# Optimization experiments

Hardware: AMD Instinct MI355X
Metric: run time of the kernel (lower is better)

Reference implementation:

```python
import jax, jax.numpy as jnp
import numpy as np

B, S, P, E, H = 2, 2048, 2048, 1024, 16
DH = E // H  # 64


def setup_inputs() -> dict:
    key = jax.random.key(0)
    ks = jax.random.split(key, 9)
    query = jax.random.normal(ks[0], (B, S, E), jnp.float32)
    key_in = jax.random.normal(ks[1], (B, S, E), jnp.float32)
    value = jax.random.normal(ks[2], (B, S, E), jnp.float32)
    past_k = jax.random.normal(ks[3], (B, H, P, DH), jnp.float32)
    past_v = jax.random.normal(ks[4], (B, H, P, DH), jnp.float32)
    # additive causal mask over the current block; all past positions visible
    i = jnp.arange(S)[:, None]          # query positions within current block
    j = jnp.arange(P + S)[None, :]      # absolute key positions
    causal = (j <= i + P)
    attn_mask = jnp.where(causal, 0.0, -1e9).astype(jnp.float32)[None, None]  # [1,1,S,P+S]
    sc = 1.0 / np.sqrt(E)
    Wq = jax.random.normal(ks[5], (E, E), jnp.float32) * sc
    Wk = jax.random.normal(ks[6], (E, E), jnp.float32) * sc
    Wv = jax.random.normal(ks[7], (E, E), jnp.float32) * sc
    Wo = jax.random.normal(ks[8], (E, E), jnp.float32) * sc
    return {"query": query, "key": key_in, "value": value,
            "past_k": past_k, "past_v": past_v, "attn_mask": attn_mask,
            "Wq": Wq, "Wk": Wk, "Wv": Wv, "Wo": Wo}


def _split_heads(x):
    # [B, S, E] -> [B, H, S, DH]  (matches view + transpose(1,2))
    b, s, _ = x.shape
    return x.reshape(b, s, H, DH).transpose(0, 2, 1, 3)


def reference(query, key, value, past_k, past_v, attn_mask, Wq, Wk, Wv, Wo):
    q = _split_heads(query @ Wq.T)          # [B,H,S,DH]
    k_new = _split_heads(key @ Wk.T)        # [B,H,S,DH]
    v_new = _split_heads(value @ Wv.T)      # [B,H,S,DH]
    k = jnp.concatenate([past_k, k_new], axis=2)   # [B,H,T,DH], T=P+S
    v = jnp.concatenate([past_v, v_new], axis=2)
    scores = jnp.einsum('bhse,bhte->bhst', q, k) / np.sqrt(DH)
    scores = scores + attn_mask
    attn = jax.nn.softmax(scores, axis=-1)
    out = jnp.einsum('bhst,bhtd->bshd', attn, v)    # [B,S,H,DH]
    out = out.reshape(query.shape[0], -1, E)         # [B,S,E]
    return out @ Wo.T
```

## Files before the change

kernel.cpp:

```cpp
#include <hip/hip_runtime.h>

#define BB 2
#define SS 2048
#define PP 2048
#define TT 4096
#define EE 1024
#define HH 16
#define DH 64

typedef __attribute__((ext_vector_type(8))) __bf16 bf16x8;
typedef __attribute__((ext_vector_type(4))) __bf16 bf16x4;
typedef __attribute__((ext_vector_type(4))) float f32x4;
typedef __attribute__((ext_vector_type(16))) float f32x16;

__device__ __forceinline__ void gload_lds16(const void* g, void* l) {
  __builtin_amdgcn_global_load_lds(
      (const __attribute__((address_space(1))) void*)g,
      (__attribute__((address_space(3))) void*)l, 16, 0, 0);
}

#define MFMA16(a, b, c) __builtin_amdgcn_mfma_f32_16x16x32_bf16((a), (b), (c), 0, 0, 0)
#define MFMA32(a, b, c) __builtin_amdgcn_mfma_f32_32x32x16_bf16((a), (b), (c), 0, 0, 0)

__device__ __forceinline__ unsigned cvtpk_bf16(float lo, float hi) {
  unsigned r;
  asm("v_cvt_pk_bf16_f32 %0, %1, %2" : "=v"(r) : "v"(lo), "v"(hi));
  return r;
}

struct ConvDesc {
  const float* s[8];
  __bf16* d[8];
  int n4[8];
};

__global__ __launch_bounds__(256) void convert_and_transpose(ConvDesc cd,
                                                             const float* __restrict__ pv,
                                                             __bf16* __restrict__ vt) {
  if (blockIdx.y < 8) {
    const int a = blockIdx.y;
    const float* __restrict__ src = cd.s[a];
    __bf16* __restrict__ dst = cd.d[a];
    const int n4 = cd.n4[a];
    const int stride = gridDim.x * blockDim.x;
    for (int i = blockIdx.x * blockDim.x + threadIdx.x; i < n4; i += stride) {
      float4 v = ((const float4*)src)[i];
      bf16x4 o = {(__bf16)v.x, (__bf16)v.y, (__bf16)v.z, (__bf16)v.w};
      ((bf16x4*)dst)[i] = o;
    }
  } else {
    __shared__ float tile[64][65];
    const int bh = blockIdx.x >> 5;
    const int k0 = (blockIdx.x & 31) * 64;
    const int tx = threadIdx.x & 63, ty = threadIdx.x >> 6;
#pragma unroll
    for (int i = 0; i < 16; ++i) {
      const int r = ty + i * 4;
      tile[r][tx] = pv[((size_t)bh * PP + k0 + r) * DH + tx];
    }
    __syncthreads();
#pragma unroll
    for (int i = 0; i < 16; ++i) {
      const int d = ty + i * 4;
      vt[((size_t)bh * DH + d) * TT + k0 + tx] = (__bf16)tile[tx][d];
    }
  }
}

__device__ __forceinline__ void gemm_core(const __bf16* A, const __bf16* Bt, __bf16* As,
                                          __bf16* Bs, int m0, int n0, f32x4 acc[4][4]) {
  const int tid = threadIdx.x, w = tid >> 6, lane = tid & 63;
  const int l15 = lane & 15, lg = lane >> 4;
  const int wr = w >> 1, wc = w & 1;
  const int cidx = w * 128 + lane;
  const int r0 = cidx >> 2, c0 = cidx & 3;
  const int r1 = r0 + 16;
  for (int kt = 0; kt < 32; ++kt) {
    const int k0 = kt * 32;
    if (kt) __syncthreads();
    gload_lds16(A + (size_t)(m0 + r0) * EE + k0 + c0 * 8, As + w * 1024);
    gload_lds16(A + (size_t)(m0 + r1) * EE + k0 + c0 * 8, As + w * 1024 + 512);
    gload_lds16(Bt + (size_t)(n0 + r0) * EE + k0 + c0 * 8, Bs + w * 1024);
    gload_lds16(Bt + (size_t)(n0 + r1) * EE + k0 + c0 * 8, Bs + w * 1024 + 512);
    __syncthreads();
    bf16x8 af[4], bf[4];
#pragma unroll
    for (int mi = 0; mi < 4; ++mi)
      af[mi] = *(const bf16x8*)&As[(wr * 64 + mi * 16 + l15) * 32 + lg * 8];
#pragma unroll
    for (int ni = 0; ni < 4; ++ni)
      bf[ni] = *(const bf16x8*)&Bs[(wc * 64 + ni * 16 + l15) * 32 + lg * 8];
#pragma unroll
    for (int mi = 0; mi < 4; ++mi)
#pragma unroll
      for (int ni = 0; ni < 4; ++ni) acc[mi][ni] = MFMA16(af[mi], bf[ni], acc[mi][ni]);
  }
}

__global__ __launch_bounds__(256) void proj_qkv(
    const __bf16* __restrict__ xq, const __bf16* __restrict__ xk, const __bf16* __restrict__ xv,
    const __bf16* __restrict__ wqb, const __bf16* __restrict__ wkb, const __bf16* __restrict__ wvb,
    __bf16* __restrict__ qws, __bf16* __restrict__ kproj, __bf16* __restrict__ vt) {
  __shared__ alignas(16) __bf16 As[4096];
  __shared__ alignas(16) __bf16 Bs[4096];
  const int z = blockIdx.z;
  const __bf16* A = (z == 0) ? xq : (z == 1) ? xk : xv;
  const __bf16* Bt = (z == 0) ? wqb : (z == 1) ? wkb : wvb;
  const int m0 = blockIdx.y * 128, n0 = blockIdx.x * 128;
  f32x4 acc[4][4];
  const f32x4 fz = {0.f, 0.f, 0.f, 0.f};
#pragma unroll
  for (int mi = 0; mi < 4; ++mi)
#pragma unroll
    for (int ni = 0; ni < 4; ++ni) acc[mi][ni] = fz;
  gemm_core(A, Bt, As, Bs, m0, n0, acc);

  const int tid = threadIdx.x, w = tid >> 6, lane = tid & 63;
  const int l15 = lane & 15, lg = lane >> 4;
  const int wr = w >> 1, wc = w & 1;
  if (z < 2) {
    __bf16* dst = (z == 0) ? qws : kproj;
    const float sc = (z == 0) ? 0.180336884f : 1.0f;
#pragma unroll
    for (int mi = 0; mi < 4; ++mi)
#pragma unroll
      for (int ni = 0; ni < 4; ++ni) {
        const int mb = m0 + wr * 64 + mi * 16 + lg * 4;
        const int n = n0 + wc * 64 + ni * 16 + l15;
#pragma unroll
        for (int r = 0; r < 4; ++r)
          dst[(size_t)(mb + r) * EE + n] = (__bf16)(acc[mi][ni][r] * sc);
      }
  } else {
#pragma unroll
    for (int mi = 0; mi < 4; ++mi)
#pragma unroll
      for (int ni = 0; ni < 4; ++ni) {
        const int mb = m0 + wr * 64 + mi * 16 + lg * 4;
        const int n = n0 + wc * 64 + ni * 16 + l15;
        const int bb = mb >> 11, s = mb & (SS - 1);
        const int hh = n >> 6, dd = n & 63;
        bf16x4 pk = {(__bf16)acc[mi][ni][0], (__bf16)acc[mi][ni][1], (__bf16)acc[mi][ni][2],
                     (__bf16)acc[mi][ni][3]};
        *(bf16x4*)&vt[((size_t)(bb * HH + hh) * DH + dd) * TT + PP + s] = pk;
      }
  }
}

__global__ __launch_bounds__(256) void gemm_out(const __bf16* __restrict__ A,
                                                const __bf16* __restrict__ Bt,
                                                float* __restrict__ C) {
  __shared__ alignas(16) __bf16 As[4096];
  __shared__ alignas(16) __bf16 Bs[4096];
  const int m0 = blockIdx.y * 128, n0 = blockIdx.x * 128;
  f32x4 acc[4][4];
  const f32x4 fz = {0.f, 0.f, 0.f, 0.f};
#pragma unroll
  for (int mi = 0; mi < 4; ++mi)
#pragma unroll
    for (int ni = 0; ni < 4; ++ni) acc[mi][ni] = fz;
  gemm_core(A, Bt, As, Bs, m0, n0, acc);

  const int tid = threadIdx.x, w = tid >> 6, lane = tid & 63;
  const int l15 = lane & 15, lg = lane >> 4;
  const int wr = w >> 1, wc = w & 1;
#pragma unroll
  for (int mi = 0; mi < 4; ++mi)
#pragma unroll
    for (int ni = 0; ni < 4; ++ni) {
      const int mb = m0 + wr * 64 + mi * 16 + lg * 4;
      const int n = n0 + wc * 64 + ni * 16 + l15;
#pragma unroll
      for (int r = 0; r < 4; ++r) C[(size_t)(mb + r) * EE + n] = acc[mi][ni][r];
    }
}

__global__ __launch_bounds__(512) void attn_kernel(const __bf16* __restrict__ q_ws,
                                                   const __bf16* __restrict__ kpast,
                                                   const __bf16* __restrict__ kproj,
                                                   const __bf16* __restrict__ vt,
                                                   __bf16* __restrict__ o0,
                                                   __bf16* __restrict__ o1,
                                                   float2* __restrict__ stats) {
  __shared__ alignas(16) __bf16 lds[3][2][4096];

  const int tid = threadIdx.x;
  const int w = tid >> 6, lane = tid & 63;
  const int l31 = lane & 31, hi = lane >> 5, l7 = lane & 7;

  const int bh = blockIdx.y;
  const int half = blockIdx.z;
  const int qb2 = half ? (7 - blockIdx.x) : blockIdx.x;
  const int b = bh >> 4, h = bh & 15;
  const int i0 = qb2 * 256;
  const int qw0 = i0 + w * 32;

  const int nt = 4 * qb2 + 36;
  const int tstart = half ? (nt >> 1) : 0;
  const int tend = half ? nt : (nt >> 1);

  const float NEGM = -12.0f;

  bf16x8 qf[4];
  {
    const __bf16* qbase = q_ws + (size_t)(b * SS + qw0 + l31) * EE + h * DH + hi * 8;
#pragma unroll
    for (int c = 0; c < 4; ++c) qf[c] = *(const bf16x8*)(qbase + 16 * c);
  }

  f32x16 oacc[2];
#pragma unroll
  for (int r = 0; r < 16; ++r) {
    oacc[0][r] = 0.f;
    oacc[1][r] = 0.f;
  }
  float l_run = 0.f;

  const int srow = tid >> 3;
  const int scg = (tid & 7) ^ (srow & 7);

  const __bf16* kp = kpast + ((size_t)bh * PP + tstart * 64 + srow) * DH + scg * 8;
  const __bf16* kn =
      kproj + (ptrdiff_t)(b * SS - PP + tstart * 64 + srow) * EE + h * DH + scg * 8;
  const __bf16* vp = vt + ((size_t)bh * DH + srow) * TT + tstart * 64 + scg * 8;

#define STAGE(buf, T)                                  \
  {                                                    \
    gload_lds16(((T) < 32) ? kp : kn, &lds[buf][0][w * 512]); \
    gload_lds16(vp, &lds[buf][1][w * 512]);            \
    kp += 64 * DH;                                     \
    kn += (ptrdiff_t)64 * EE;                          \
    vp += 64;                                          \
  }

#define ITER(T, CUR, NXT)                                                                \
  {                                                                                      \
    if ((T) + 1 < tend) {                                                                \
      asm volatile("s_waitcnt vmcnt(2)" ::: "memory");        \
    } else {                                                                             \
      asm volatile("s_waitcnt vmcnt(0)" ::: "memory");        \
    }                                                                                    \
    __builtin_amdgcn_s_barrier();  \
    if ((T) + 2 < tend) STAGE(NXT, (T) + 2);                                             \
    const int kv0 = (T)*64;                                                              \
    if (kv0 <= qw0 + 31 + PP) {                             \
      f32x16 p[2];                                                                       \
      _Pragma("unroll") for (int s = 0; s < 2; ++s)                                      \
      _Pragma("unroll") for (int r = 0; r < 16; ++r) p[s][r] = NEGM;                     \
      const __bf16* Kb = lds[CUR][0];                                                    \
      __builtin_amdgcn_s_setprio(1);                                                     \
      _Pragma("unroll") for (int s = 0; s < 2; ++s)                                      \
      _Pragma("unroll") for (int c = 0; c < 4; ++c) {                                    \
        const bf16x8 kf =                                                                \
            *(const bf16x8*)&Kb[(32 * s + l31) * 64 + (((2 * c + hi) ^ l7) << 3)];       \
        p[s] = MFMA32(kf, qf[c], p[s]);                                                  \
      }                                                                                  \
      __builtin_amdgcn_s_setprio(0);                                                     \
      if (kv0 + 63 > qw0 + PP) {                                                         \
        const int qa = qw0 + l31 + PP;                                                   \
        _Pragma("unroll") for (int s = 0; s < 2; ++s)                                    \
        _Pragma("unroll") for (int r = 0; r < 16; ++r) {                                 \
          const int key = kv0 + 32 * s + (r & 3) + 8 * (r >> 2) + 4 * hi;                \
          if (key > qa) p[s][r] = -1e30f;                                                \
        }                                                                                \
      }                                                                                  \
      _Pragma("unroll") for (int s = 0; s < 2; ++s)                                      \
      _Pragma("unroll") for (int r = 0; r < 16; ++r)                                     \
          p[s][r] = __builtin_amdgcn_exp2f(p[s][r]);                                     \
      float s16[16];                                                                     \
      _Pragma("unroll") for (int r = 0; r < 16; ++r) s16[r] = p[0][r] + p[1][r];         \
      _Pragma("unroll") for (int st = 8; st > 0; st >>= 1)                               \
      _Pragma("unroll") for (int r = 0; r < st; ++r) s16[r] += s16[r + st];              \
      l_run += s16[0] + __shfl_xor(s16[0], 32, 64);                                      \
      bf16x8 pb[4];                                                                      \
      _Pragma("unroll") for (int s = 0; s < 2; ++s)                                      \
      _Pragma("unroll") for (int u = 0; u < 2; ++u) {                                    \
        unsigned a0 = cvtpk_bf16(p[s][8 * u + 0], p[s][8 * u + 1]);                      \
        unsigned a1 = cvtpk_bf16(p[s][8 * u + 2], p[s][8 * u + 3]);                      \
        unsigned b0 = cvtpk_bf16(p[s][8 * u + 4], p[s][8 * u + 5]);                      \
        unsigned b1 = cvtpk_bf16(p[s][8 * u + 6], p[s][8 * u + 7]);                      \
        asm volatile("v_permlane32_swap_b32 %0, %1" : "+v"(a0), "+v"(b0));               \
        asm volatile("v_permlane32_swap_b32 %0, %1" : "+v"(a1), "+v"(b1));               \
        union {                                                                          \
          unsigned u32[4];                                                               \
          bf16x8 v;                                                                      \
        } pk;                                                                            \
        pk.u32[0] = a0;                                                                  \
        pk.u32[1] = a1;                                                                  \
        pk.u32[2] = b0;                                                                  \
        pk.u32[3] = b1;                                                                  \
        pb[2 * s + u] = pk.v;                                                            \
      }                                                                                  \
      const __bf16* Vb = lds[CUR][1];                                                    \
      __builtin_amdgcn_s_setprio(1);                                                     \
      _Pragma("unroll") for (int u = 0; u < 4; ++u) {                                    \
        const bf16x8 vf0 = *(const bf16x8*)&Vb[l31 * 64 + (((2 * u + hi) ^ l7) << 3)];   \
        oacc[0] = MFMA32(vf0, pb[u], oacc[0]);                                           \
        const bf16x8 vf1 =                                                               \
            *(const bf16x8*)&Vb[(32 + l31) * 64 + (((2 * u + hi) ^ l7) << 3)];           \
        oacc[1] = MFMA32(vf1, pb[u], oacc[1]);                                           \
      }                                                                                  \
      __builtin_amdgcn_s_setprio(0);                                                     \
    }                                                                                    \
  }

  STAGE(0, tstart);
  if (tstart + 1 < tend) STAGE(1, tstart + 1);

  const int ntp = tend - tstart;
  int j = 0;
  for (; j + 3 <= ntp; j += 3) {
    ITER(tstart + j, 0, 2);
    ITER(tstart + j + 1, 1, 0);
    ITER(tstart + j + 2, 2, 1);
  }
  if (j < ntp) ITER(tstart + j, 0, 2);
  if (j + 1 < ntp) ITER(tstart + j + 1, 1, 0);

  const float inv = 1.0f / l_run;
  __bf16* od = half ? o1 : o0;
  const size_t orow = (size_t)(b * SS + qw0 + l31) * EE + h * DH;
#pragma unroll
  for (int dblk = 0; dblk < 2; ++dblk)
#pragma unroll
    for (int g = 0; g < 4; ++g) {
      bf16x4 v4;
#pragma unroll
      for (int r4 = 0; r4 < 4; ++r4) v4[r4] = (__bf16)(oacc[dblk][4 * g + r4] * inv);
      *(bf16x4*)&od[orow + 32 * dblk + 8 * g + 4 * hi] = v4;
    }
  if (hi == 0) {
    stats[((size_t)half * (BB * SS) + b * SS + qw0 + l31) * HH + h] = float2{12.0f, l_run};
  }
#undef ITER
#undef STAGE
}

__global__ __launch_bounds__(256) void combine_halves(const __bf16* __restrict__ o0,
                                                      const __bf16* __restrict__ o1,
                                                      const float2* __restrict__ st,
                                                      __bf16* __restrict__ ao) {
  const int tid = threadIdx.x;
  const int row = blockIdx.x * 2 + (tid >> 7);
  const int c8 = tid & 127;
  const int h = c8 >> 3;
  const float2 s0 = st[(size_t)row * HH + h];
  const float2 s1 = st[(size_t)(BB * SS + row) * HH + h];
  const float m = fmaxf(s0.x, s1.x);
  float w0 = __builtin_amdgcn_exp2f(s0.x - m) * s0.y;
  float w1 = __builtin_amdgcn_exp2f(s1.x - m) * s1.y;
  const float inv = 1.0f / (w0 + w1);
  w0 *= inv;
  w1 *= inv;
  const size_t off = (size_t)row * EE + c8 * 8;
  const bf16x8 a = *(const bf16x8*)(o0 + off);
  const bf16x8 b = *(const bf16x8*)(o1 + off);
  bf16x8 o;
#pragma unroll
  for (int r = 0; r < 8; ++r) o[r] = (__bf16)(w0 * (float)a[r] + w1 * (float)b[r]);
  *(bf16x8*)(ao + off) = o;
}

extern "C" void kernel_launch(void* const* d_in, const int* in_sizes, int n_in, void* d_out,
                              int out_size, void* d_ws, size_t ws_size, hipStream_t stream) {
  const float* query = (const float*)d_in[0];
  const float* key_in = (const float*)d_in[1];
  const float* value = (const float*)d_in[2];
  const float* past_k = (const float*)d_in[3];
  const float* past_v = (const float*)d_in[4];
  const float* Wq = (const float*)d_in[6];
  const float* Wk = (const float*)d_in[7];
  const float* Wv = (const float*)d_in[8];
  const float* Wo = (const float*)d_in[9];

  char* ws = (char*)d_ws;
  __bf16* XQ = (__bf16*)(ws + 0);
  __bf16* XK = (__bf16*)(ws + 8388608);
  __bf16* XV = (__bf16*)(ws + 16777216);
  __bf16* WQB = (__bf16*)(ws + 25165824);
  __bf16* WKB = (__bf16*)(ws + 27262976);
  __bf16* WVB = (__bf16*)(ws + 29360128);
  __bf16* WOB = (__bf16*)(ws + 31457280);
  __bf16* QW = (__bf16*)(ws + 33554432);
  __bf16* KP = (__bf16*)(ws + 41943040);
  __bf16* KN = (__bf16*)(ws + 50331648);
  __bf16* VT = (__bf16*)(ws + 58720256);
  float2* ST = (float2*)(ws + 0);
  __bf16* O1 = (__bf16*)(ws + 2097152);
  __bf16* O0 = (__bf16*)(ws + 75497472);
  __bf16* AO = QW;

  ConvDesc cd;
  cd.s[0] = query;  cd.d[0] = XQ;  cd.n4[0] = 1048576;
  cd.s[1] = key_in; cd.d[1] = XK;  cd.n4[1] = 1048576;
  cd.s[2] = value;  cd.d[2] = XV;  cd.n4[2] = 1048576;
  cd.s[3] = Wq;     cd.d[3] = WQB; cd.n4[3] = 262144;
  cd.s[4] = Wk;     cd.d[4] = WKB; cd.n4[4] = 262144;
  cd.s[5] = Wv;     cd.d[5] = WVB; cd.n4[5] = 262144;
  cd.s[6] = Wo;     cd.d[6] = WOB; cd.n4[6] = 262144;
  cd.s[7] = past_k; cd.d[7] = KP;  cd.n4[7] = 1048576;

  convert_and_transpose<<<dim3(1024, 9, 1), 256, 0, stream>>>(cd, past_v, VT);
  proj_qkv<<<dim3(8, 32, 3), 256, 0, stream>>>(XQ, XK, XV, WQB, WKB, WVB, QW, KN, VT);
  attn_kernel<<<dim3(8, 32, 2), 512, 0, stream>>>(QW, KP, KN, VT, O0, O1, ST);
  combine_halves<<<dim3(2048, 1, 1), 256, 0, stream>>>(O0, O1, ST, AO);
  gemm_out<<<dim3(8, 32, 1), 256, 0, stream>>>(AO, WOB, (float*)d_out);
}
```

Measured before the change: 155.9 us.

## Rewrite QKV projection GEMM as 256x256 double-buffered swizzled pipelined kernel

Replaces the 128x128 single-buffered QKV projection GEMM with a 256x256 tile kernel using 512 threads, BK=64, double-buffered LDS with XOR-swizzled layout, and interleaved global-to-LDS staging across MFMA phases with setprio. The goal is to hide global load latency behind MFMA work, cut LDS bank conflicts and raise data reuse per tile. The trade-off is fewer blocks (192) on a 256-CU device, so parts of the chip may sit idle, plus heavier register and LDS use (128KB LDS per block).

Measured after the change: 154.4 us, median of 4. Within noise of the previous version (-1.0%).

```diff
diff --git a/kernel.cpp b/kernel.cpp
--- a/kernel.cpp
+++ b/kernel.cpp
@@ -97,51 +97,133 @@
   }
 }
 
-__global__ __launch_bounds__(256) void proj_qkv(
+__global__ __launch_bounds__(512, 2) void proj_qkv256(
     const __bf16* __restrict__ xq, const __bf16* __restrict__ xk, const __bf16* __restrict__ xv,
     const __bf16* __restrict__ wqb, const __bf16* __restrict__ wkb, const __bf16* __restrict__ wvb,
     __bf16* __restrict__ qws, __bf16* __restrict__ kproj, __bf16* __restrict__ vt) {
-  __shared__ alignas(16) __bf16 As[4096];
-  __shared__ alignas(16) __bf16 Bs[4096];
+  __shared__ alignas(16) __bf16 As[2][16384];
+  __shared__ alignas(16) __bf16 Bs[2][16384];
+
+  const int tid = threadIdx.x;
+  const int w = tid >> 6, lane = tid & 63;
+  const int l15 = lane & 15, lg = (lane >> 4) & 3;
+  const int wm = w >> 2, wn = w & 3;
+
   const int z = blockIdx.z;
   const __bf16* A = (z == 0) ? xq : (z == 1) ? xk : xv;
   const __bf16* Bt = (z == 0) ? wqb : (z == 1) ? wkb : wvb;
-  const int m0 = blockIdx.y * 128, n0 = blockIdx.x * 128;
-  f32x4 acc[4][4];
+  const int m0 = blockIdx.y * 256, n0 = blockIdx.x * 256;
+
+  f32x4 acc[8][4];
   const f32x4 fz = {0.f, 0.f, 0.f, 0.f};
 #pragma unroll
-  for (int mi = 0; mi < 4; ++mi)
-#pragma unroll
-    for (int ni = 0; ni < 4; ++ni) acc[mi][ni] = fz;
-  gemm_core(A, Bt, As, Bs, m0, n0, acc);
-
-  const int tid = threadIdx.x, w = tid >> 6, lane = tid & 63;
-  const int l15 = lane & 15, lg = lane >> 4;
-  const int wr = w >> 1, wc = w & 1;
+  for (int mf = 0; mf < 8; ++mf)
+#pragma unroll
+    for (int nf = 0; nf < 4; ++nf) acc[mf][nf] = fz;
+
+  const int srow = lane >> 3;
+  const int scg = (lane & 7) ^ srow;
+  const __bf16* baseA = A + (size_t)(m0 + w * 8 + srow) * EE + scg * 8;
+  const __bf16* baseB = Bt + (size_t)(n0 + w * 8 + srow) * EE + scg * 8;
+
+  const int rowA = wm * 128 + l15;
+  const int rowB = wn * 64 + l15;
+  const int swz = l15 & 7;
+  const int aoff0 = (lg ^ swz) << 3;
+  const int aoff1 = ((4 + lg) ^ swz) << 3;
+
+#define STGH(BUF, BASE, HALF, KT)                                                         \
+  {                                                                                       \
+    gload_lds16((BASE) + (size_t)((HALF)*128) * EE + (size_t)(KT)*64,                     \
+                &(BUF)[(((HALF)*128) + w * 8) * 64]);                                     \
+    gload_lds16((BASE) + (size_t)((HALF)*128 + 64) * EE + (size_t)(KT)*64,                \
+                &(BUF)[(((HALF)*128 + 64) + w * 8) * 64]);                                \
+  }
+
+#define LOADB(CUR)                                                                        \
+  _Pragma("unroll") for (int nf = 0; nf < 4; ++nf) {                                      \
+    bfr[2 * nf] = *(const bf16x8*)&Bs[CUR][(rowB + nf * 16) * 64 + aoff0];                \
+    bfr[2 * nf + 1] = *(const bf16x8*)&Bs[CUR][(rowB + nf * 16) * 64 + aoff1];            \
+  }
+
+#define PHASE(CUR, MB, STAGECODE, VMCODE)                                                 \
+  {                                                                                       \
+    afr[0] = *(const bf16x8*)&As[CUR][(rowA + (MB)*16) * 64 + aoff0];                     \
+    afr[1] = *(const bf16x8*)&As[CUR][(rowA + (MB)*16) * 64 + aoff1];                     \
+    afr[2] = *(const bf16x8*)&As[CUR][(rowA + (MB)*16 + 16) * 64 + aoff0];                \
+    afr[3] = *(const bf16x8*)&As[CUR][(rowA + (MB)*16 + 16) * 64 + aoff1];                \
+    STAGECODE;                                                                            \
+    __builtin_amdgcn_s_barrier();                                                         \
+    __builtin_amdgcn_s_setprio(1);                                                        \
+    _Pragma("unroll") for (int nf = 0; nf < 4; ++nf) {                                    \
+      acc[MB][nf] = MFMA16(afr[0], bfr[2 * nf], acc[MB][nf]);                             \
+      acc[MB][nf] = MFMA16(afr[1], bfr[2 * nf + 1], acc[MB][nf]);                         \
+      acc[(MB) + 1][nf] = MFMA16(afr[2], bfr[2 * nf], acc[(MB) + 1][nf]);                 \
+      acc[(MB) + 1][nf] = MFMA16(afr[3], bfr[2 * nf + 1], acc[(MB) + 1][nf]);             \
+    }                                                                                     \
+    __builtin_amdgcn_s_setprio(0);                                                        \
+    VMCODE;                                                                               \
+    __builtin_amdgcn_s_barrier();                                                         \
+  }
+
+  STGH(As[0], baseA, 0, 0);
+  STGH(As[0], baseA, 1, 0);
+  STGH(Bs[0], baseB, 0, 0);
+  STGH(Bs[0], baseB, 1, 0);
+  STGH(Bs[1], baseB, 0, 1);
+  STGH(Bs[1], baseB, 1, 1);
+  asm volatile("s_waitcnt vmcnt(4)" ::: "memory");
+  __builtin_amdgcn_s_barrier();
+
+  for (int i = 0; i < 8; ++i) {
+    const int kt1 = 2 * i + 1, kt2 = 2 * i + 2, kt3 = 2 * i + 3;
+    const bool st = (i < 7);
+    bf16x8 bfr[8], afr[4];
+    LOADB(0);
+    PHASE(0, 0, { STGH(As[1], baseA, 0, kt1); }, {});
+    PHASE(0, 2, { STGH(As[1], baseA, 1, kt1); }, {});
+    PHASE(0, 4, { if (st) STGH(Bs[0], baseB, 0, kt2); }, {});
+    PHASE(0, 6, { if (st) STGH(Bs[0], baseB, 1, kt2); }, {
+      if (st) { asm volatile("s_waitcnt vmcnt(4)" ::: "memory"); }
+      else    { asm volatile("s_waitcnt vmcnt(0)" ::: "memory"); }
+    });
+    LOADB(1);
+    PHASE(1, 0, { if (st) STGH(As[0], baseA, 0, kt2); }, {});
+    PHASE(1, 2, { if (st) STGH(As[0], baseA, 1, kt2); }, {});
+    PHASE(1, 4, { if (st) STGH(Bs[1], baseB, 0, kt3); }, {});
+    PHASE(1, 6, { if (st) STGH(Bs[1], baseB, 1, kt3); }, {
+      if (st) { asm volatile("s_waitcnt vmcnt(4)" ::: "memory"); }
+      else    { asm volatile("s_waitcnt vmcnt(0)" ::: "memory"); }
+    });
+  }
+#undef PHASE
+#undef LOADB
+#undef STGH
+
   if (z < 2) {
     __bf16* dst = (z == 0) ? qws : kproj;
     const float sc = (z == 0) ? 0.180336884f : 1.0f;
 #pragma unroll
-    for (int mi = 0; mi < 4; ++mi)
-#pragma unroll
-      for (int ni = 0; ni < 4; ++ni) {
-        const int mb = m0 + wr * 64 + mi * 16 + lg * 4;
-        const int n = n0 + wc * 64 + ni * 16 + l15;
+    for (int mf = 0; mf < 8; ++mf)
+#pragma unroll
+      for (int nf = 0; nf < 4; ++nf) {
+        const int mb = m0 + wm * 128 + mf * 16 + lg * 4;
+        const int n = n0 + wn * 64 + nf * 16 + l15;
 #pragma unroll
         for (int r = 0; r < 4; ++r)
-          dst[(size_t)(mb + r) * EE + n] = (__bf16)(acc[mi][ni][r] * sc);
+          dst[(size_t)(mb + r) * EE + n] = (__bf16)(acc[mf][nf][r] * sc);
       }
   } else {
 #pragma unroll
-    for (int mi = 0; mi < 4; ++mi)
-#pragma unroll
-      for (int ni = 0; ni < 4; ++ni) {
-        const int mb = m0 + wr * 64 + mi * 16 + lg * 4;
-        const int n = n0 + wc * 64 + ni * 16 + l15;
+    for (int mf = 0; mf < 8; ++mf)
+#pragma unroll
+      for (int nf = 0; nf < 4; ++nf) {
+        const int mb = m0 + wm * 128 + mf * 16 + lg * 4;
+        const int n = n0 + wn * 64 + nf * 16 + l15;
         const int bb = mb >> 11, s = mb & (SS - 1);
         const int hh = n >> 6, dd = n & 63;
-        bf16x4 pk = {(__bf16)acc[mi][ni][0], (__bf16)acc[mi][ni][1], (__bf16)acc[mi][ni][2],
-                     (__bf16)acc[mi][ni][3]};
+        bf16x4 pk = {(__bf16)acc[mf][nf][0], (__bf16)acc[mf][nf][1], (__bf16)acc[mf][nf][2],
+                     (__bf16)acc[mf][nf][3]};
         *(bf16x4*)&vt[((size_t)(bb * HH + hh) * DH + dd) * TT + PP + s] = pk;
       }
   }
@@ -401,7 +483,7 @@
   cd.s[7] = past_k; cd.d[7] = KP;  cd.n4[7] = 1048576;
 
   convert_and_transpose<<<dim3(1024, 9, 1), 256, 0, stream>>>(cd, past_v, VT);
-  proj_qkv<<<dim3(8, 32, 3), 256, 0, stream>>>(XQ, XK, XV, WQB, WKB, WVB, QW, KN, VT);
+  proj_qkv256<<<dim3(4, 16, 3), 512, 0, stream>>>(XQ, XK, XV, WQB, WKB, WVB, QW, KN, VT);
   attn_kernel<<<dim3(8, 32, 2), 512, 0, stream>>>(QW, KP, KN, VT, O0, O1, ST);
   combine_halves<<<dim3(2048, 1, 1), 256, 0, stream>>>(O0, O1, ST, AO);
   gemm_out<<<dim3(8, 32, 1), 256, 0, stream>>>(AO, WOB, (float*)d_out);
```
